# Optimization experiments

Measured on AMD Instinct MI355X. Metric: run time of the kernel, lower is better.

## Reference

```python
import jax, jax.numpy as jnp
import numpy as np

N_NODES = 100000
DROP_P = 0.2


def _degree_norm(idx, n):
    deg = jax.ops.segment_sum(jnp.ones_like(idx, dtype=jnp.float32), idx, num_segments=n)
    return jnp.maximum(deg, 1.0) ** -0.5


def gcn_layer(x, src, dst, W, b, n):
    # DGL GraphConv, norm='both', in_feats > out_feats so weight is applied first.
    norm_src = _degree_norm(src, n)  # out-degree^{-1/2}
    norm_dst = _degree_norm(dst, n)  # in-degree^{-1/2}
    h = (x * norm_src[:, None]) @ W            # [N, d_out]
    agg = jax.ops.segment_sum(h[src], dst, num_segments=n)  # gather-scatter over edges
    return agg * norm_dst[:, None] + b


def setup_inputs() -> dict:
    key = jax.random.key(0)
    k = jax.random.split(key, 5)
    x = jax.random.normal(k[0], (N_NODES, 256), dtype=jnp.float32)
    edge_index = jax.random.randint(k[1], (2, 1600000), 0, N_NODES, dtype=jnp.int64)
    W1 = jax.random.normal(k[2], (256, 128), dtype=jnp.float32) * (1.0 / np.sqrt(256))
    b1 = jnp.zeros((128,), dtype=jnp.float32)
    W2 = jax.random.normal(k[3], (128, 47), dtype=jnp.float32) * (1.0 / np.sqrt(128))
    b2 = jnp.zeros((47,), dtype=jnp.float32)
    return {"x": x, "edge_index": edge_index, "W1": W1, "b1": b1, "W2": W2, "b2": b2}


def reference(x, edge_index, W1, b1, W2, b2):
    src, dst = edge_index[0], edge_index[1]
    n = x.shape[0]
    # CRD: GraphConv -> relu -> dropout (F.dropout default training=True; fixed mask)
    h = gcn_layer(x, src, dst, W1, b1, n)
    h = jax.nn.relu(h)
    keep = jax.random.bernoulli(jax.random.key(42), 1.0 - DROP_P, h.shape)
    h = jnp.where(keep, h / (1.0 - DROP_P), 0.0)
    # CLS: GraphConv -> log_softmax over class dim
    out = gcn_layer(h, src, dst, W2, b2, n)
    return jax.nn.log_softmax(out, axis=-1)
```

## Files before the change

### kernel.cpp

```cpp
#include <hip/hip_runtime.h>
#include <math.h>


#define NF0 256
#define NF1 128
#define NC  47
#define CB  1024

typedef __attribute__((ext_vector_type(8))) short bfrag;
typedef __attribute__((ext_vector_type(4))) float f32x4;

__device__ __forceinline__ unsigned short f2bf(float f) {
  unsigned u = __float_as_uint(f);
  return (unsigned short)((u + 0x7fffu + ((u >> 16) & 1u)) >> 16);
}
__device__ __forceinline__ unsigned pack2bf(float a, float b) {
  return (unsigned)f2bf(a) | ((unsigned)f2bf(b) << 16);
}
__device__ __forceinline__ float bflo(unsigned v) { return __uint_as_float(v << 16); }
__device__ __forceinline__ float bfhi(unsigned v) { return __uint_as_float(v & 0xffff0000u); }
__device__ __forceinline__ float bf2f(unsigned short b) {
  return __uint_as_float((unsigned)b << 16);
}

__device__ __forceinline__ unsigned rotl_(unsigned x, int n) {
  return (x << n) | (x >> (32 - n));
}
__device__ __forceinline__ void threefry2x32_(unsigned x0, unsigned x1,
                                              unsigned& o0, unsigned& o1) {
  const unsigned k0 = 0u, k1 = 42u;
  const unsigned k2 = k0 ^ k1 ^ 0x1BD11BDAu;
  x0 += k0; x1 += k1;
  x0+=x1; x1=rotl_(x1,13); x1^=x0;
  x0+=x1; x1=rotl_(x1,15); x1^=x0;
  x0+=x1; x1=rotl_(x1,26); x1^=x0;
  x0+=x1; x1=rotl_(x1, 6); x1^=x0;
  x0+=k1; x1+=k2+1u;
  x0+=x1; x1=rotl_(x1,17); x1^=x0;
  x0+=x1; x1=rotl_(x1,29); x1^=x0;
  x0+=x1; x1=rotl_(x1,16); x1^=x0;
  x0+=x1; x1=rotl_(x1,24); x1^=x0;
  x0+=k2; x1+=k0+2u;
  x0+=x1; x1=rotl_(x1,13); x1^=x0;
  x0+=x1; x1=rotl_(x1,15); x1^=x0;
  x0+=x1; x1=rotl_(x1,26); x1^=x0;
  x0+=x1; x1=rotl_(x1, 6); x1^=x0;
  x0+=k0; x1+=k1+3u;
  x0+=x1; x1=rotl_(x1,17); x1^=x0;
  x0+=x1; x1=rotl_(x1,29); x1^=x0;
  x0+=x1; x1=rotl_(x1,16); x1^=x0;
  x0+=x1; x1=rotl_(x1,24); x1^=x0;
  x0+=k1; x1+=k2+4u;
  x0+=x1; x1=rotl_(x1,13); x1^=x0;
  x0+=x1; x1=rotl_(x1,15); x1^=x0;
  x0+=x1; x1=rotl_(x1,26); x1^=x0;
  x0+=x1; x1=rotl_(x1, 6); x1^=x0;
  x0+=k2; x1+=k0+5u;
  o0 = x0; o1 = x1;
}
__device__ __forceinline__ float dropout_mul(int j) {
  unsigned o0, o1;
  threefry2x32_(0u, (unsigned)j, o0, o1);
  unsigned bits = o0 ^ o1;
  float u = __uint_as_float((bits >> 9) | 0x3f800000u) - 1.0f;
  return (u < 0.8f) ? 1.25f : 0.0f;
}


__global__ __launch_bounds__(256) void k_chist(const int* __restrict__ ei, int E,
                                               int nbk,
                                               unsigned* __restrict__ bCntD,
                                               unsigned* __restrict__ bCntS,
                                               const float* __restrict__ W1,
                                               const float* __restrict__ W2,
                                               unsigned* __restrict__ W1t32,
                                               unsigned* __restrict__ W2t32) {
  if (blockIdx.x >= 256) {
    int i = (blockIdx.x - 256) * 256 + threadIdx.x;
    if (i < 128 * 128) {
      int n = i >> 7, k = (i & 127) << 1;
      W1t32[i] = pack2bf(W1[(size_t)k * NF1 + n], W1[(size_t)(k + 1) * NF1 + n]);
    } else if (i < 128 * 128 + 48 * 64) {
      int j = i - 128 * 128;
      int f = j >> 6, k = (j & 63) << 1;
      float a = (f < NC) ? W2[(size_t)k * NC + f] : 0.f;
      float c = (f < NC) ? W2[(size_t)(k + 1) * NC + f] : 0.f;
      W2t32[j] = pack2bf(a, c);
    }
    return;
  }
  __shared__ unsigned hd[128], hs[128];
  for (int i = threadIdx.x; i < 128; i += 256) { hd[i] = 0; hs[i] = 0; }
  __syncthreads();
  for (int e = blockIdx.x * 256 + threadIdx.x; e < E; e += 256 * 256) {
    int s = ei[e], d = ei[E + e];
    atomicAdd(&hs[s >> 10], 1u);
    atomicAdd(&hd[d >> 10], 1u);
  }
  __syncthreads();
  for (int i = threadIdx.x; i < nbk; i += 256) {
    if (hd[i]) atomicAdd(&bCntD[i], hd[i]);
    if (hs[i]) atomicAdd(&bCntS[i], hs[i]);
  }
}

__global__ __launch_bounds__(256) void k_cscatter(const int* __restrict__ ei, int E,
                                                  const unsigned* __restrict__ bCntD,
                                                  const unsigned* __restrict__ bCntS,
                                                  unsigned* __restrict__ curD,
                                                  unsigned* __restrict__ curS,
                                                  unsigned* __restrict__ pd,
                                                  unsigned short* __restrict__ ps,
                                                  int nbk) {
  __shared__ unsigned hd[128], hs[128];
  __shared__ unsigned baseD[128], baseS[128];
  __shared__ unsigned sc[256];
  const int t = threadIdx.x;
  int per = (E + gridDim.x - 1) / gridDim.x;
  int e0 = blockIdx.x * per;
  int e1 = min(e0 + per, E);
  unsigned orig = (t < 128) ? ((t < nbk) ? bCntD[t] : 0u)
                            : (((t - 128) < nbk) ? bCntS[t - 128] : 0u);
  sc[t] = orig;
  if (t < 128) { hd[t] = 0; hs[t] = 0; }
  __syncthreads();
  for (int e = e0 + t; e < e1; e += 256) {
    int s = ei[e], d = ei[E + e];
    atomicAdd(&hs[s >> 10], 1u);
    atomicAdd(&hd[d >> 10], 1u);
  }
  __syncthreads();
  #pragma unroll
  for (int o = 1; o < 128; o <<= 1) {
    unsigned u = ((t & 127) >= o) ? sc[t - o] : 0u;
    __syncthreads();
    sc[t] += u;
    __syncthreads();
  }
  if (t < 128) {
    unsigned excl = sc[t] - orig;
    unsigned h = hd[t];
    baseD[t] = excl + (h ? atomicAdd(&curD[t], h) : 0u);
    hd[t] = 0;
  } else {
    int i = t - 128;
    unsigned excl = sc[t] - orig;
    unsigned h = hs[i];
    baseS[i] = excl + (h ? atomicAdd(&curS[i], h) : 0u);
    hs[i] = 0;
  }
  __syncthreads();
  for (int e = e0 + t; e < e1; e += 256) {
    int s = ei[e], d = ei[E + e];
    int bd = d >> 10, bs = s >> 10;
    unsigned pD = baseD[bd] + atomicAdd(&hd[bd], 1u);
    unsigned pS = baseS[bs] + atomicAdd(&hs[bs], 1u);
    pd[pD] = ((unsigned)(d & (CB - 1)) << 17) | (unsigned)s;
    ps[pS] = (unsigned short)(s & (CB - 1));
  }
}

__global__ __launch_bounds__(256) void k_fine(const unsigned* __restrict__ bCntD,
                                              const unsigned* __restrict__ bCntS,
                                              const unsigned* __restrict__ pd,
                                              const unsigned short* __restrict__ ps,
                                              unsigned* __restrict__ off,
                                              float* __restrict__ norm_dst,
                                              float* __restrict__ norm_src,
                                              int* __restrict__ csr,
                                              int N, int E, int nbk) {
  __shared__ unsigned cnt[CB];
  __shared__ unsigned part[256];
  __shared__ unsigned sc[256];
  const int t = threadIdx.x;
  const bool isD = (int)blockIdx.x < nbk;
  const int b = isD ? (int)blockIdx.x : ((int)blockIdx.x - nbk);
  unsigned orig = (t < 128) ? ((t < nbk) ? bCntD[t] : 0u)
                            : (((t - 128) < nbk) ? bCntS[t - 128] : 0u);
  sc[t] = orig;
  __syncthreads();
  #pragma unroll
  for (int o = 1; o < 128; o <<= 1) {
    unsigned u = ((t & 127) >= o) ? sc[t - o] : 0u;
    __syncthreads();
    sc[t] += u;
    __syncthreads();
  }
  const int idx = isD ? b : (128 + b);
  const unsigned hi = sc[idx];
  const unsigned lo = hi - (isD ? bCntD[b] : bCntS[b]);
  const int base = b << 10;
  for (int i = t; i < CB; i += 256) cnt[i] = 0;
  __syncthreads();
  if (isD) {
    for (unsigned j = lo + t; j < hi; j += 256) atomicAdd(&cnt[pd[j] >> 17], 1u);
    __syncthreads();
    unsigned c0 = cnt[4*t], c1 = cnt[4*t+1], c2 = cnt[4*t+2], c3 = cnt[4*t+3];
    unsigned tsum = c0 + c1 + c2 + c3;
    part[t] = tsum;
    __syncthreads();
    #pragma unroll
    for (int o = 1; o < 256; o <<= 1) {
      unsigned u = (t >= o) ? part[t - o] : 0u;
      __syncthreads();
      part[t] += u;
      __syncthreads();
    }
    unsigned e0 = part[t] - tsum;
    unsigned p0 = e0, p1 = e0 + c0, p2 = p1 + c1, p3 = p2 + c2;
    int n0 = base + 4 * t;
    if (n0 + 0 < N) { off[n0+0] = lo + p0; norm_dst[n0+0] = 1.0f / sqrtf((float)(c0 < 1u ? 1u : c0)); }
    if (n0 + 1 < N) { off[n0+1] = lo + p1; norm_dst[n0+1] = 1.0f / sqrtf((float)(c1 < 1u ? 1u : c1)); }
    if (n0 + 2 < N) { off[n0+2] = lo + p2; norm_dst[n0+2] = 1.0f / sqrtf((float)(c2 < 1u ? 1u : c2)); }
    if (n0 + 3 < N) { off[n0+3] = lo + p3; norm_dst[n0+3] = 1.0f / sqrtf((float)(c3 < 1u ? 1u : c3)); }
    if (b == nbk - 1 && t == 0) off[N] = (unsigned)E;
    __syncthreads();
    cnt[4*t] = p0; cnt[4*t+1] = p1; cnt[4*t+2] = p2; cnt[4*t+3] = p3;
    __syncthreads();
    for (unsigned j = lo + t; j < hi; j += 256) {
      unsigned v = pd[j];
      unsigned pos = atomicAdd(&cnt[v >> 17], 1u);
      csr[lo + pos] = (int)(v & 0x1FFFFu);
    }
  } else {
    for (unsigned j = lo + t; j < hi; j += 256) atomicAdd(&cnt[ps[j]], 1u);
    __syncthreads();
    for (int i = t; i < CB; i += 256) {
      int n = base + i;
      if (n < N) {
        unsigned c = cnt[i];
        norm_src[n] = 1.0f / sqrtf((float)(c < 1u ? 1u : c));
      }
    }
  }
}

__global__ __launch_bounds__(256) void k_gemm1(const float* __restrict__ x,
                                               const unsigned* __restrict__ W1t32,
                                               const float* __restrict__ norm_src,
                                               unsigned short* __restrict__ h1, int N) {
  __shared__ unsigned As[128][20];
  __shared__ unsigned Bs[128][20];
  const int m0 = blockIdx.x * 128;
  const int t = threadIdx.x;
  const int lane = t & 63, wid = t >> 6;
  const int fr = lane & 15, ko = (lane >> 4) * 8;

  f32x4 acc[2][8];
  #pragma unroll
  for (int r = 0; r < 2; r++)
    #pragma unroll
    for (int c = 0; c < 8; c++) acc[r][c] = (f32x4){0.f, 0.f, 0.f, 0.f};

  const int sr = t >> 1;
  const int shw = (t & 1) * 8;

  for (int k0 = 0; k0 < NF0; k0 += 32) {
    {
      unsigned w[8];
      int gm = m0 + sr;
      if (gm < N) {
        const float* p = x + (size_t)gm * NF0 + k0 + shw * 2;
        #pragma unroll
        for (int q = 0; q < 4; q++) {
          float4 v = *(const float4*)(p + q * 4);
          w[2*q]   = pack2bf(v.x, v.y);
          w[2*q+1] = pack2bf(v.z, v.w);
        }
      } else {
        #pragma unroll
        for (int q = 0; q < 8; q++) w[q] = 0u;
      }
      *(uint4*)&As[sr][shw]     = make_uint4(w[0], w[1], w[2], w[3]);
      *(uint4*)&As[sr][shw + 4] = make_uint4(w[4], w[5], w[6], w[7]);
    }
    {
      const unsigned* pb = W1t32 + (size_t)sr * (NF0 / 2) + (k0 >> 1) + shw;
      *(uint4*)&Bs[sr][shw]     = *(const uint4*)pb;
      *(uint4*)&Bs[sr][shw + 4] = *(const uint4*)(pb + 4);
    }
    __syncthreads();
    const unsigned short* As16 = (const unsigned short*)&As[0][0];
    const unsigned short* Bs16 = (const unsigned short*)&Bs[0][0];
    #pragma unroll
    for (int r = 0; r < 2; r++) {
      bfrag a = *(const bfrag*)(As16 + (size_t)(wid * 32 + r * 16 + fr) * 40 + ko);
      #pragma unroll
      for (int c = 0; c < 8; c++) {
        bfrag b = *(const bfrag*)(Bs16 + (size_t)(c * 16 + fr) * 40 + ko);
        acc[r][c] = __builtin_amdgcn_mfma_f32_16x16x32_bf16(a, b, acc[r][c], 0, 0, 0);
      }
    }
    __syncthreads();
  }

  #pragma unroll
  for (int r = 0; r < 2; r++) {
    int rbase = m0 + wid * 32 + r * 16 + (lane >> 4) * 4;
    float ns[4];
    #pragma unroll
    for (int g = 0; g < 4; g++) ns[g] = (rbase + g < N) ? norm_src[rbase + g] : 0.f;
    #pragma unroll
    for (int c = 0; c < 8; c++) {
      int col = c * 16 + fr;
      #pragma unroll
      for (int g = 0; g < 4; g++) {
        int row = rbase + g;
        if (row < N) h1[(size_t)row * NF1 + col] = f2bf(acc[r][c][g] * ns[g]);
      }
    }
  }
}

#define G2PAD 70
__global__ __launch_bounds__(256) void k_g1g2(const unsigned* __restrict__ off,
                                              const int* __restrict__ csr,
                                              const unsigned short* __restrict__ h1,
                                              const float* __restrict__ norm_dst,
                                              const float* __restrict__ norm_src,
                                              const float* __restrict__ b1,
                                              const unsigned* __restrict__ W2t32,
                                              unsigned short* __restrict__ g, int N) {
  __shared__ unsigned hsb[64 * G2PAD];
  const int t = threadIdx.x;
  const int m0 = blockIdx.x * 64;
  const int lane = t & 63, wid = t >> 6;
  const int f = lane << 1;

  for (int nn = 0; nn < 16; nn++) {
    int lrow = wid * 16 + nn;
    int node = m0 + lrow;
    if (node >= N) break;
    unsigned j = off[node], e1 = off[node + 1];
    float ax = 0.f, ay = 0.f;
    for (; j + 4 <= e1; j += 4) {
      int s0 = csr[j], s1 = csr[j+1], s2 = csr[j+2], s3 = csr[j+3];
      unsigned v0 = *(const unsigned*)(h1 + (size_t)s0 * NF1 + f);
      unsigned v1 = *(const unsigned*)(h1 + (size_t)s1 * NF1 + f);
      unsigned v2 = *(const unsigned*)(h1 + (size_t)s2 * NF1 + f);
      unsigned v3 = *(const unsigned*)(h1 + (size_t)s3 * NF1 + f);
      ax += (bflo(v0) + bflo(v1)) + (bflo(v2) + bflo(v3));
      ay += (bfhi(v0) + bfhi(v1)) + (bfhi(v2) + bfhi(v3));
    }
    for (; j < e1; j++) {
      unsigned v = *(const unsigned*)(h1 + (size_t)csr[j] * NF1 + f);
      ax += bflo(v); ay += bfhi(v);
    }
    float nd = norm_dst[node], ns = norm_src[node];
    float2 bb = *(const float2*)(b1 + f);
    float v0 = fmaxf(ax * nd + bb.x, 0.f);
    float v1 = fmaxf(ay * nd + bb.y, 0.f);
    int jf = node * NF1 + f;
    v0 *= dropout_mul(jf) * ns;
    v1 *= dropout_mul(jf + 1) * ns;
    hsb[lrow * G2PAD + lane] = pack2bf(v0, v1);
  }
  __syncthreads();

  const int fg = t & 15, mg = t >> 4;
  const int f0 = fg * 3, mt = mg * 4;
  float acc[4][3] = {{0.f}};
  for (int k = 0; k < NF1; k += 4) {
    float a[4][4];
    #pragma unroll
    for (int i = 0; i < 4; i++) {
      uint2 u = *(const uint2*)&hsb[(mt + i) * G2PAD + (k >> 1)];
      a[i][0] = bflo(u.x); a[i][1] = bfhi(u.x);
      a[i][2] = bflo(u.y); a[i][3] = bfhi(u.y);
    }
    float bv[3][4];
    #pragma unroll
    for (int jj = 0; jj < 3; jj++) {
      uint2 u = *(const uint2*)(W2t32 + (size_t)(f0 + jj) * 64 + (k >> 1));
      bv[jj][0] = bflo(u.x); bv[jj][1] = bfhi(u.x);
      bv[jj][2] = bflo(u.y); bv[jj][3] = bfhi(u.y);
    }
    #pragma unroll
    for (int i = 0; i < 4; i++)
      #pragma unroll
      for (int jj = 0; jj < 3; jj++)
        acc[i][jj] += a[i][0]*bv[jj][0] + a[i][1]*bv[jj][1]
                    + a[i][2]*bv[jj][2] + a[i][3]*bv[jj][3];
  }
  #pragma unroll
  for (int i = 0; i < 4; i++) {
    int gm = m0 + mt + i;
    if (gm < N) {
      #pragma unroll
      for (int jj = 0; jj < 3; jj++)
        g[(size_t)gm * 48 + f0 + jj] = f2bf(acc[i][jj]);
    }
  }
}

__global__ __launch_bounds__(256) void k_gather2(const unsigned* __restrict__ off,
                                                 const int* __restrict__ csr,
                                                 const unsigned short* __restrict__ g,
                                                 const float* __restrict__ norm_dst,
                                                 const float* __restrict__ b2,
                                                 float* __restrict__ out, int N) {
  int node = (blockIdx.x * 256 + threadIdx.x) >> 6;
  int lane = threadIdx.x & 63;
  if (node >= N) return;
  unsigned j = off[node], e1 = off[node + 1];
  float acc = 0.f;
  for (; j + 4 <= e1; j += 4) {
    int s0 = csr[j], s1 = csr[j+1], s2 = csr[j+2], s3 = csr[j+3];
    if (lane < 48) {
      float a0 = bf2f(g[(size_t)s0 * 48 + lane]);
      float a1 = bf2f(g[(size_t)s1 * 48 + lane]);
      float a2 = bf2f(g[(size_t)s2 * 48 + lane]);
      float a3 = bf2f(g[(size_t)s3 * 48 + lane]);
      acc += (a0 + a1) + (a2 + a3);
    }
  }
  for (; j < e1; j++) {
    if (lane < 48) acc += bf2f(g[(size_t)csr[j] * 48 + lane]);
  }
  float nd = norm_dst[node];
  float vr = 0.f, m = -INFINITY;
  if (lane < NC) {
    vr = acc * nd + b2[lane];
    m = vr;
  }
  #pragma unroll
  for (int o = 32; o; o >>= 1) m = fmaxf(m, __shfl_xor(m, o));
  float ex = (lane < NC) ? expf(vr - m) : 0.f;
  #pragma unroll
  for (int o = 32; o; o >>= 1) ex += __shfl_xor(ex, o);
  float ls = logf(ex);
  if (lane < NC) out[(size_t)node * NC + lane] = vr - m - ls;
}

extern "C" void kernel_launch(void* const* d_in, const int* in_sizes, int n_in,
                              void* d_out, int out_size, void* d_ws, size_t ws_size,
                              hipStream_t stream) {
  const float* x  = (const float*)d_in[0];
  const int*   ei = (const int*)d_in[1];
  const float* W1 = (const float*)d_in[2];
  const float* b1 = (const float*)d_in[3];
  const float* W2 = (const float*)d_in[4];
  const float* b2 = (const float*)d_in[5];
  float* out = (float*)d_out;

  const int N = in_sizes[0] / NF0;
  const int E = in_sizes[1] / 2;
  const int nbk = (N + CB - 1) / CB;

  unsigned* ws = (unsigned*)d_ws;
  size_t o = 0;
  auto alloc = [&](size_t elems) { size_t p = o; o += (elems + 3) & ~(size_t)3; return p; };
  float*    norm_src = (float*)(ws + alloc(N));
  float*    norm_dst = (float*)(ws + alloc(N));
  unsigned* off      = ws + alloc(N + 1);
  unsigned* bCntD    = ws + alloc(128);
  unsigned* bCntS    = ws + alloc(128);
  unsigned* curD     = ws + alloc(128);
  unsigned* curS     = ws + alloc(128);
  unsigned* pd       = ws + alloc(E);
  unsigned short* ps = (unsigned short*)(ws + alloc(E / 2));
  int*      csr      = (int*)(ws + alloc(E));
  unsigned* W1t32    = ws + alloc(128 * 128);
  unsigned* W2t32    = ws + alloc(48 * 64);
  unsigned short* h1 = (unsigned short*)(ws + alloc((size_t)N * NF1 / 2));
  unsigned short* gbuf;
  if ((size_t)E * 3 >= (size_t)N * 48) {
    gbuf = (unsigned short*)pd;
  } else {
    gbuf = (unsigned short*)(ws + alloc(((size_t)N * 48 + 1) / 2));
  }

  hipMemsetAsync(bCntD, 0, 512 * sizeof(unsigned), stream);

  int wblk = (128 * 128 + 48 * 64 + 255) / 256;
  k_chist<<<256 + wblk, 256, 0, stream>>>(ei, E, nbk, bCntD, bCntS, W1, W2, W1t32, W2t32);
  k_cscatter<<<256, 256, 0, stream>>>(ei, E, bCntD, bCntS, curD, curS, pd, ps, nbk);
  k_fine<<<2 * nbk, 256, 0, stream>>>(bCntD, bCntS, pd, ps, off, norm_dst, norm_src,
                                      csr, N, E, nbk);
  k_gemm1<<<(N + 127) / 128, 256, 0, stream>>>(x, W1t32, norm_src, h1, N);
  k_g1g2<<<(N + 63) / 64, 256, 0, stream>>>(off, csr, h1, norm_dst, norm_src, b1,
                                            W2t32, gbuf, N);
  k_gather2<<<((size_t)N * 64 + 255) / 256, 256, 0, stream>>>(
      off, csr, gbuf, norm_dst, b2, out, N);
}
```

Measured before the change: 518.4 us.

## Restructure layer-2 fusion as persistent per-wave gather plus row matvec

```diff
diff --git a/kernel.cpp b/kernel.cpp
--- a/kernel.cpp
+++ b/kernel.cpp
@@ -312,7 +312,7 @@
   }
 }
 
-#define G2PAD 70
+#define W2STR 66
 __global__ __launch_bounds__(256) void k_g1g2(const unsigned* __restrict__ off,
                                               const int* __restrict__ csr,
                                               const unsigned short* __restrict__ h1,
@@ -321,16 +321,23 @@
                                               const float* __restrict__ b1,
                                               const unsigned* __restrict__ W2t32,
                                               unsigned short* __restrict__ g, int N) {
-  __shared__ unsigned hsb[64 * G2PAD];
+  __shared__ unsigned W2L[48 * W2STR];
+  __shared__ unsigned row[4 * 64];
   const int t = threadIdx.x;
-  const int m0 = blockIdx.x * 64;
   const int lane = t & 63, wid = t >> 6;
+  for (int i = t; i < 48 * 64; i += 256) {
+    W2L[(i >> 6) * W2STR + (i & 63)] = W2t32[i];
+  }
+  __syncthreads();
+
   const int f = lane << 1;
-
-  for (int nn = 0; nn < 16; nn++) {
-    int lrow = wid * 16 + nn;
-    int node = m0 + lrow;
-    if (node >= N) break;
+  unsigned* rp = &row[wid * 64];
+  const unsigned* wp = &W2L[lane * W2STR];
+  const int ngroups = (N + 3) >> 2;
+
+  for (int grp = blockIdx.x; grp < ngroups; grp += gridDim.x) {
+    int node = grp * 4 + wid;
+    if (node >= N) continue;
     unsigned j = off[node], e1 = off[node + 1];
     float ax = 0.f, ay = 0.f;
     for (; j + 4 <= e1; j += 4) {
@@ -353,43 +360,20 @@
     int jf = node * NF1 + f;
     v0 *= dropout_mul(jf) * ns;
     v1 *= dropout_mul(jf + 1) * ns;
-    hsb[lrow * G2PAD + lane] = pack2bf(v0, v1);
-  }
-  __syncthreads();
-
-  const int fg = t & 15, mg = t >> 4;
-  const int f0 = fg * 3, mt = mg * 4;
-  float acc[4][3] = {{0.f}};
-  for (int k = 0; k < NF1; k += 4) {
-    float a[4][4];
-    #pragma unroll
-    for (int i = 0; i < 4; i++) {
-      uint2 u = *(const uint2*)&hsb[(mt + i) * G2PAD + (k >> 1)];
-      a[i][0] = bflo(u.x); a[i][1] = bfhi(u.x);
-      a[i][2] = bflo(u.y); a[i][3] = bfhi(u.y);
-    }
-    float bv[3][4];
-    #pragma unroll
-    for (int jj = 0; jj < 3; jj++) {
-      uint2 u = *(const uint2*)(W2t32 + (size_t)(f0 + jj) * 64 + (k >> 1));
-      bv[jj][0] = bflo(u.x); bv[jj][1] = bfhi(u.x);
-      bv[jj][2] = bflo(u.y); bv[jj][3] = bfhi(u.y);
-    }
-    #pragma unroll
-    for (int i = 0; i < 4; i++)
+    rp[lane] = pack2bf(v0, v1);
+    __builtin_amdgcn_wave_barrier();
+    if (lane < 48) {
+      float acc = 0.f;
       #pragma unroll
-      for (int jj = 0; jj < 3; jj++)
-        acc[i][jj] += a[i][0]*bv[jj][0] + a[i][1]*bv[jj][1]
-                    + a[i][2]*bv[jj][2] + a[i][3]*bv[jj][3];
-  }
-  #pragma unroll
-  for (int i = 0; i < 4; i++) {
-    int gm = m0 + mt + i;
-    if (gm < N) {
-      #pragma unroll
-      for (int jj = 0; jj < 3; jj++)
-        g[(size_t)gm * 48 + f0 + jj] = f2bf(acc[i][jj]);
-    }
+      for (int kp = 0; kp < 64; kp += 2) {
+        uint2 u = *(const uint2*)(rp + kp);
+        uint2 w = *(const uint2*)(wp + kp);
+        acc += bflo(u.x) * bflo(w.x) + bfhi(u.x) * bfhi(w.x)
+             + bflo(u.y) * bflo(w.y) + bfhi(u.y) * bfhi(w.y);
+      }
+      g[(size_t)node * 48 + lane] = f2bf(acc);
+    }
+    __builtin_amdgcn_wave_barrier();
   }
 }
 
@@ -478,8 +462,8 @@
   k_fine<<<2 * nbk, 256, 0, stream>>>(bCntD, bCntS, pd, ps, off, norm_dst, norm_src,
                                       csr, N, E, nbk);
   k_gemm1<<<(N + 127) / 128, 256, 0, stream>>>(x, W1t32, norm_src, h1, N);
-  k_g1g2<<<(N + 63) / 64, 256, 0, stream>>>(off, csr, h1, norm_dst, norm_src, b1,
-                                            W2t32, gbuf, N);
+  k_g1g2<<<2048, 256, 0, stream>>>(off, csr, h1, norm_dst, norm_src, b1,
+                                   W2t32, gbuf, N);
   k_gather2<<<((size_t)N * 64 + 255) / 256, 256, 0, stream>>>(
       off, csr, gbuf, norm_dst, b2, out, N);
 }
```

After: 495.6 us. -4.4%, faster.
